# Performance work log

Measured on AMD Instinct MI355X. Metric: run time of the kernel, lower is better.

## Reference

```python
import jax, jax.numpy as jnp
import numpy as np

N_NODES = 100000
N_EDGES = 1600000
F_IN = 256
F_OUT = 32


def setup_inputs() -> dict:
    key = jax.random.key(0)
    k1, k2, k3 = jax.random.split(key, 3)
    x = jax.random.normal(k1, (N_NODES, F_IN), dtype=jnp.float32)
    edge_index = jax.random.randint(k2, (2, N_EDGES), 0, N_NODES, dtype=jnp.int64)
    W = jax.random.normal(k3, (F_IN, F_OUT), dtype=jnp.float32) / np.sqrt(F_IN)
    b = jnp.zeros((F_OUT,), dtype=jnp.float32)
    return {"x": x, "edge_index": edge_index, "W": W, "b": b}


def reference(x, edge_index, W, b):
    # PyG GCNConv: add self-loops, symmetric normalization, linear, aggregate.
    N = x.shape[0]
    loop = jnp.arange(N, dtype=edge_index.dtype)
    src = jnp.concatenate([edge_index[0], loop])  # message sources
    dst = jnp.concatenate([edge_index[1], loop])  # aggregation targets

    deg = jax.ops.segment_sum(jnp.ones_like(dst, dtype=x.dtype), dst,
                              num_segments=N)
    deg_inv_sqrt = jnp.where(deg > 0, jax.lax.rsqrt(jnp.maximum(deg, 1.0)), 0.0)
    norm = deg_inv_sqrt[src] * deg_inv_sqrt[dst]  # [E+N]

    h = x @ W  # [N, F_OUT] transform first (as PyG does)
    msg = h[src] * norm[:, None]  # gather + scale
    out = jax.ops.segment_sum(msg, dst, num_segments=N) + b
    return out
```

## Files before the change

### kernel.cpp

```cpp
#include <hip/hip_runtime.h>

#define F_IN  256
#define F_OUT 32

#define NPB       512
#define NPB_SHIFT 9
#define NB2MAX    256
#define EPW       8192
#define BCAP      10240

typedef __attribute__((ext_vector_type(8))) short bf16x8;
typedef __attribute__((ext_vector_type(4))) float f32x4;

__device__ __forceinline__ short f2bf(float f) {
    unsigned u = __float_as_uint(f);
    u += 0x7FFF + ((u >> 16) & 1);
    return (short)(u >> 16);
}

__global__ __launch_bounds__(256) void k_zero(int* __restrict__ bcur,
                                              const int* __restrict__ ei,
                                              int* __restrict__ flag) {
    int i = blockIdx.x * 256 + threadIdx.x;
    if (i < NB2MAX) bcur[i] = i * BCAP;
    if (i == 0) {
        int o = 0;
        for (int k = 1; k < 64; k += 2) o |= ei[k];
        *flag = (o == 0) ? 1 : 0;
    }
}

__global__ __launch_bounds__(512) void k_bucket(const int* __restrict__ ei,
                                                const int* __restrict__ flag,
                                                int* __restrict__ bcur,
                                                int* __restrict__ ebuf,
                                                int E, int N) {
    __shared__ int lhist[NB2MAX];
    __shared__ int lbase[NB2MAX];
    __shared__ int sP[EPW];
    __shared__ unsigned short sB[EPW];
    const int tid = threadIdx.x;
    if (tid < NB2MAX) lhist[tid] = 0;
    __syncthreads();
    const int m64 = *flag;
    const long long e0 = (long long)blockIdx.x * EPW;
    #pragma unroll 4
    for (int j = 0; j < EPW / 512; ++j) {
        int idx = j * 512 + tid;
        long long e = e0 + idx;
        unsigned short bb = 0xFFFF;
        int pk = 0;
        if (e < E) {
            int s, d;
            if (m64) { s = ei[2 * (size_t)e]; d = ei[2 * ((size_t)E + e)]; }
            else     { s = ei[(size_t)e];     d = ei[(size_t)E + e]; }
            if ((unsigned)d < (unsigned)N && (unsigned)s < (unsigned)N) {
                bb = (unsigned short)(d >> NPB_SHIFT);
                pk = s | ((d & (NPB - 1)) << 23);
                atomicAdd(&lhist[bb], 1);
            }
        }
        sB[idx] = bb;
        sP[idx] = pk;
    }
    __syncthreads();
    if (tid < NB2MAX) {
        int c = lhist[tid];
        lbase[tid] = c ? atomicAdd(&bcur[tid], c) : 0;
        lhist[tid] = 0;
    }
    __syncthreads();
    #pragma unroll 4
    for (int j = 0; j < EPW / 512; ++j) {
        int idx = j * 512 + tid;
        unsigned short bb = sB[idx];
        if (bb != 0xFFFF) {
            int slot = lbase[bb] + atomicAdd(&lhist[bb], 1);
            if (slot < (int)(bb + 1) * BCAP) ebuf[slot] = sP[idx];
        }
    }
}

__global__ __launch_bounds__(1024) void k_sort(int* __restrict__ ebuf,
                                               const int* __restrict__ bcur,
                                               float* __restrict__ dinv,
                                               int* __restrict__ offp, int N) {
    __shared__ int sedge[BCAP];
    __shared__ int lcnt[NPB];
    __shared__ int lofs[NPB];
    __shared__ int sc[NPB];
    const int tid = threadIdx.x;
    const int b = blockIdx.x;
    const int start = b * BCAP;
    const int m = min(max(bcur[b] - start, 0), BCAP);

    for (int i = tid; i < m; i += 1024) sedge[i] = ebuf[start + i];
    if (tid < NPB) lcnt[tid] = 0;
    __syncthreads();
    for (int i = tid; i < m; i += 1024)
        atomicAdd(&lcnt[((unsigned)sedge[i]) >> 23], 1);
    __syncthreads();
    int c0 = (tid < NPB) ? lcnt[tid] : 0;
    int val = c0;
    if (tid < NPB) sc[tid] = val;
    __syncthreads();
    #pragma unroll
    for (int d2 = 1; d2 < NPB; d2 <<= 1) {
        int t = (tid < NPB && tid >= d2) ? sc[tid - d2] : 0;
        __syncthreads();
        if (tid < NPB) { val += t; sc[tid] = val; }
        __syncthreads();
    }
    if (tid < NPB) {
        int excl = val - c0;
        lofs[tid] = excl;
        int n = (b << NPB_SHIFT) + tid;
        if (n < N) {
            dinv[n] = rsqrtf((float)c0 + 1.0f);
            offp[n] = (start + excl) | (min(c0, 1023) << 22);
        }
    }
    __syncthreads();
    for (int i = tid; i < m; i += 1024) {
        int pk = sedge[i];
        int l = ((unsigned)pk) >> 23;
        int slot = start + atomicAdd(&lofs[l], 1);
        ebuf[slot] = pk & 0x7FFFFF;
    }
}

#define WLDP 264
__global__ __launch_bounds__(256) void k_gemm(const float* __restrict__ x,
                                              const float* __restrict__ W,
                                              const float* __restrict__ dinv,
                                              _Float16* __restrict__ hs16, int N) {
    __shared__ __align__(16) short sWt[F_OUT * WLDP];
    const int tid = threadIdx.x;
    const int lane = tid & 63;
    const int wave = tid >> 6;
    const int row0 = blockIdx.x * 128 + wave * 32;

    for (int i = tid; i < F_IN * F_OUT; i += 256) {
        int f = i & 31, k = i >> 5;
        sWt[f * WLDP + k] = f2bf(W[i]);
    }
    __syncthreads();

    const int l15 = lane & 15;
    const int lg  = lane >> 4;
    int ra = row0 + l15;
    int rb = row0 + 16 + l15;
    int rac = min(ra, N - 1);
    int rbc = min(rb, N - 1);

    const float* xa = x + (size_t)rac * F_IN + lg * 8;
    const float* xb = x + (size_t)rbc * F_IN + lg * 8;
    const short* wb0 = sWt + l15 * WLDP + lg * 8;
    const short* wb1 = sWt + (16 + l15) * WLDP + lg * 8;

    f32x4 acc00 = {0.f, 0.f, 0.f, 0.f};
    f32x4 acc01 = {0.f, 0.f, 0.f, 0.f};
    f32x4 acc10 = {0.f, 0.f, 0.f, 0.f};
    f32x4 acc11 = {0.f, 0.f, 0.f, 0.f};

    #pragma unroll
    for (int kb = 0; kb < F_IN / 32; ++kb) {
        float4 a0 = *(const float4*)(xa + kb * 32);
        float4 a1 = *(const float4*)(xa + kb * 32 + 4);
        float4 b0 = *(const float4*)(xb + kb * 32);
        float4 b1 = *(const float4*)(xb + kb * 32 + 4);
        bf16x8 A0, A1;
        A0[0] = f2bf(a0.x); A0[1] = f2bf(a0.y); A0[2] = f2bf(a0.z); A0[3] = f2bf(a0.w);
        A0[4] = f2bf(a1.x); A0[5] = f2bf(a1.y); A0[6] = f2bf(a1.z); A0[7] = f2bf(a1.w);
        A1[0] = f2bf(b0.x); A1[1] = f2bf(b0.y); A1[2] = f2bf(b0.z); A1[3] = f2bf(b0.w);
        A1[4] = f2bf(b1.x); A1[5] = f2bf(b1.y); A1[6] = f2bf(b1.z); A1[7] = f2bf(b1.w);
        bf16x8 B0 = *(const bf16x8*)(wb0 + kb * 32);
        bf16x8 B1 = *(const bf16x8*)(wb1 + kb * 32);
        acc00 = __builtin_amdgcn_mfma_f32_16x16x32_bf16(A0, B0, acc00, 0, 0, 0);
        acc01 = __builtin_amdgcn_mfma_f32_16x16x32_bf16(A0, B1, acc01, 0, 0, 0);
        acc10 = __builtin_amdgcn_mfma_f32_16x16x32_bf16(A1, B0, acc10, 0, 0, 0);
        acc11 = __builtin_amdgcn_mfma_f32_16x16x32_bf16(A1, B1, acc11, 0, 0, 0);
    }

    #pragma unroll
    for (int r = 0; r < 4; ++r) {
        int row = row0 + lg * 4 + r;
        if (row < N) {
            float di = dinv[row];
            hs16[(size_t)row * F_OUT + l15]      = (_Float16)(acc00[r] * di);
            hs16[(size_t)row * F_OUT + 16 + l15] = (_Float16)(acc01[r] * di);
        }
        int row2 = row + 16;
        if (row2 < N) {
            float di2 = dinv[row2];
            hs16[(size_t)row2 * F_OUT + l15]      = (_Float16)(acc10[r] * di2);
            hs16[(size_t)row2 * F_OUT + 16 + l15] = (_Float16)(acc11[r] * di2);
        }
    }
}

__global__ __launch_bounds__(256) void k_agg(const _Float16* __restrict__ hs16,
                                             const int* __restrict__ adj,
                                             const int* __restrict__ offp,
                                             const float* __restrict__ dinv,
                                             const float* __restrict__ bias,
                                             float* __restrict__ out, int N) {
    const int tid = threadIdx.x;
    const int n = blockIdx.x * 64 + (tid >> 2);
    const int q = tid & 3;
    if (n >= N) return;

    const int po = offp[n];
    const int st = po & 0x3FFFFF;
    const int deg = ((unsigned)po) >> 22;

    const uint4* __restrict__ h4 = (const uint4*)hs16;
    union U { uint4 u; _Float16 h[8]; };

    float a[8];
    {
        U sv; sv.u = h4[(size_t)n * 4 + q];
        #pragma unroll
        for (int i = 0; i < 8; ++i) a[i] = (float)sv.h[i];
    }

    int k = 0;
    for (; k + 4 <= deg; k += 4) {
        int s0 = adj[st + k];
        int s1 = adj[st + k + 1];
        int s2 = adj[st + k + 2];
        int s3 = adj[st + k + 3];
        U v0, v1, v2, v3;
        v0.u = h4[(size_t)s0 * 4 + q];
        v1.u = h4[(size_t)s1 * 4 + q];
        v2.u = h4[(size_t)s2 * 4 + q];
        v3.u = h4[(size_t)s3 * 4 + q];
        #pragma unroll
        for (int i = 0; i < 8; ++i)
            a[i] += ((float)v0.h[i] + (float)v1.h[i]) +
                    ((float)v2.h[i] + (float)v3.h[i]);
    }
    for (; k < deg; ++k) {
        int s0 = adj[st + k];
        U v0; v0.u = h4[(size_t)s0 * 4 + q];
        #pragma unroll
        for (int i = 0; i < 8; ++i) a[i] += (float)v0.h[i];
    }

    const float di = dinv[n];
    const float4 bv0 = ((const float4*)bias)[q * 2];
    const float4 bv1 = ((const float4*)bias)[q * 2 + 1];
    float4 o0, o1;
    o0.x = bv0.x + di * a[0]; o0.y = bv0.y + di * a[1];
    o0.z = bv0.z + di * a[2]; o0.w = bv0.w + di * a[3];
    o1.x = bv1.x + di * a[4]; o1.y = bv1.y + di * a[5];
    o1.z = bv1.z + di * a[6]; o1.w = bv1.w + di * a[7];
    float4* op = (float4*)(out + (size_t)n * F_OUT);
    op[q * 2]     = o0;
    op[q * 2 + 1] = o1;
}

extern "C" void kernel_launch(void* const* d_in, const int* in_sizes, int n_in,
                              void* d_out, int out_size, void* d_ws, size_t ws_size,
                              hipStream_t stream) {
    const float* x  = (const float*)d_in[0];
    const int*   ei = (const int*)d_in[1];
    const float* W  = (const float*)d_in[2];
    const float* b  = (const float*)d_in[3];
    float* out = (float*)d_out;

    const int N = in_sizes[0] / F_IN;
    const int E = in_sizes[1] / 2;

    _Float16* hs16 = (_Float16*)d_ws;
    int*   ebuf = (int*)(hs16 + (size_t)N * F_OUT);
    float* dinv = (float*)(ebuf + (size_t)NB2MAX * BCAP);
    int*   offp = (int*)(dinv + N);
    int*   bcur = offp + N;
    int*   flag = bcur + NB2MAX;

    const int NB  = (N + NPB - 1) >> NPB_SHIFT;
    const int NBW = (int)(((long long)E + EPW - 1) / EPW);

    k_zero  <<<1, 256, 0, stream>>>(bcur, ei, flag);
    k_bucket<<<NBW, 512, 0, stream>>>(ei, flag, bcur, ebuf, E, N);
    k_sort  <<<NB, 1024, 0, stream>>>(ebuf, bcur, dinv, offp, N);
    k_gemm  <<<(N + 127) / 128, 256, 0, stream>>>(x, W, dinv, hs16, N);
    k_agg   <<<(N * 4 + 255) / 256, 256, 0, stream>>>(hs16, ebuf, offp, dinv, b, out, N);
}
```

Baseline: 231.4 us.

## Sort nodes by degree within blocks and unroll aggregation by eight

k_sort now builds a per-block counting sort of nodes by in-degree and writes a node permutation (nord). k_agg walks nodes in that order, so neighbouring threads and waves handle nodes of similar degree, which reduces loop-trip divergence inside a wave. The aggregation loop also gains an 8-wide unroll with a second accumulator set, giving more gathers in flight. The cost is an extra indirection load per node, scattered output writes, and extra scans and atomics in k_sort plus a larger k_zero launch.

```diff
diff --git a/kernel.cpp b/kernel.cpp
--- a/kernel.cpp
+++ b/kernel.cpp
@@ -8,6 +8,7 @@
 #define NB2MAX    256
 #define EPW       8192
 #define BCAP      10240
+#define DEGB      128
 
 typedef __attribute__((ext_vector_type(8))) short bf16x8;
 typedef __attribute__((ext_vector_type(4))) float f32x4;
@@ -19,10 +20,12 @@
 }
 
 __global__ __launch_bounds__(256) void k_zero(int* __restrict__ bcur,
+                                              int* __restrict__ nord,
                                               const int* __restrict__ ei,
-                                              int* __restrict__ flag) {
+                                              int* __restrict__ flag, int tot) {
     int i = blockIdx.x * 256 + threadIdx.x;
     if (i < NB2MAX) bcur[i] = i * BCAP;
+    if (i < tot) nord[i] = -1;
     if (i == 0) {
         int o = 0;
         for (int k = 1; k < 64; k += 2) o |= ei[k];
@@ -84,11 +87,14 @@
 __global__ __launch_bounds__(1024) void k_sort(int* __restrict__ ebuf,
                                                const int* __restrict__ bcur,
                                                float* __restrict__ dinv,
-                                               int* __restrict__ offp, int N) {
+                                               int* __restrict__ offp,
+                                               int* __restrict__ nord, int N) {
     __shared__ int sedge[BCAP];
     __shared__ int lcnt[NPB];
     __shared__ int lofs[NPB];
     __shared__ int sc[NPB];
+    __shared__ int dh[DEGB];
+    __shared__ int dho[DEGB];
     const int tid = threadIdx.x;
     const int b = blockIdx.x;
     const int start = b * BCAP;
@@ -96,6 +102,7 @@
 
     for (int i = tid; i < m; i += 1024) sedge[i] = ebuf[start + i];
     if (tid < NPB) lcnt[tid] = 0;
+    if (tid >= NPB && tid < NPB + DEGB) dh[tid - NPB] = 0;
     __syncthreads();
     for (int i = tid; i < m; i += 1024)
         atomicAdd(&lcnt[((unsigned)sedge[i]) >> 23], 1);
@@ -111,16 +118,37 @@
         if (tid < NPB) { val += t; sc[tid] = val; }
         __syncthreads();
     }
+    const int n = (b << NPB_SHIFT) + tid;
+    const int nvalid = (tid < NPB) && (n < N);
     if (tid < NPB) {
         int excl = val - c0;
         lofs[tid] = excl;
-        int n = (b << NPB_SHIFT) + tid;
-        if (n < N) {
+        if (nvalid) {
             dinv[n] = rsqrtf((float)c0 + 1.0f);
             offp[n] = (start + excl) | (min(c0, 1023) << 22);
         }
     }
     __syncthreads();
+    const int dg = min(c0, DEGB - 1);
+    if (nvalid) atomicAdd(&dh[dg], 1);
+    __syncthreads();
+    int dv = (tid < DEGB) ? dh[tid] : 0;
+    int dval = dv;
+    if (tid < DEGB) sc[tid] = dval;
+    __syncthreads();
+    #pragma unroll
+    for (int d2 = 1; d2 < DEGB; d2 <<= 1) {
+        int t = (tid < DEGB && tid >= d2) ? sc[tid - d2] : 0;
+        __syncthreads();
+        if (tid < DEGB) { dval += t; sc[tid] = dval; }
+        __syncthreads();
+    }
+    if (tid < DEGB) dho[tid] = dval - dv;
+    __syncthreads();
+    if (nvalid) {
+        int r = atomicAdd(&dho[dg], 1);
+        nord[(b << NPB_SHIFT) + r] = n;
+    }
     for (int i = tid; i < m; i += 1024) {
         int pk = sedge[i];
         int l = ((unsigned)pk) >> 23;
@@ -202,13 +230,16 @@
 __global__ __launch_bounds__(256) void k_agg(const _Float16* __restrict__ hs16,
                                              const int* __restrict__ adj,
                                              const int* __restrict__ offp,
+                                             const int* __restrict__ nord,
                                              const float* __restrict__ dinv,
                                              const float* __restrict__ bias,
-                                             float* __restrict__ out, int N) {
+                                             float* __restrict__ out, int N, int tot) {
     const int tid = threadIdx.x;
-    const int n = blockIdx.x * 64 + (tid >> 2);
+    const int r = blockIdx.x * 64 + (tid >> 2);
     const int q = tid & 3;
-    if (n >= N) return;
+    if (r >= tot) return;
+    const int n = nord[r];
+    if ((unsigned)n >= (unsigned)N) return;
 
     const int po = offp[n];
     const int st = po & 0x3FFFFF;
@@ -217,14 +248,40 @@
     const uint4* __restrict__ h4 = (const uint4*)hs16;
     union U { uint4 u; _Float16 h[8]; };
 
-    float a[8];
+    float a[8], c[8];
     {
         U sv; sv.u = h4[(size_t)n * 4 + q];
         #pragma unroll
-        for (int i = 0; i < 8; ++i) a[i] = (float)sv.h[i];
+        for (int i = 0; i < 8; ++i) { a[i] = (float)sv.h[i]; c[i] = 0.f; }
     }
 
     int k = 0;
+    for (; k + 8 <= deg; k += 8) {
+        int s0 = adj[st + k];
+        int s1 = adj[st + k + 1];
+        int s2 = adj[st + k + 2];
+        int s3 = adj[st + k + 3];
+        int s4 = adj[st + k + 4];
+        int s5 = adj[st + k + 5];
+        int s6 = adj[st + k + 6];
+        int s7 = adj[st + k + 7];
+        U v0, v1, v2, v3, v4, v5, v6, v7;
+        v0.u = h4[(size_t)s0 * 4 + q];
+        v1.u = h4[(size_t)s1 * 4 + q];
+        v2.u = h4[(size_t)s2 * 4 + q];
+        v3.u = h4[(size_t)s3 * 4 + q];
+        v4.u = h4[(size_t)s4 * 4 + q];
+        v5.u = h4[(size_t)s5 * 4 + q];
+        v6.u = h4[(size_t)s6 * 4 + q];
+        v7.u = h4[(size_t)s7 * 4 + q];
+        #pragma unroll
+        for (int i = 0; i < 8; ++i) {
+            a[i] += ((float)v0.h[i] + (float)v1.h[i]) +
+                    ((float)v2.h[i] + (float)v3.h[i]);
+            c[i] += ((float)v4.h[i] + (float)v5.h[i]) +
+                    ((float)v6.h[i] + (float)v7.h[i]);
+        }
+    }
     for (; k + 4 <= deg; k += 4) {
         int s0 = adj[st + k];
         int s1 = adj[st + k + 1];
@@ -251,10 +308,10 @@
     const float4 bv0 = ((const float4*)bias)[q * 2];
     const float4 bv1 = ((const float4*)bias)[q * 2 + 1];
     float4 o0, o1;
-    o0.x = bv0.x + di * a[0]; o0.y = bv0.y + di * a[1];
-    o0.z = bv0.z + di * a[2]; o0.w = bv0.w + di * a[3];
-    o1.x = bv1.x + di * a[4]; o1.y = bv1.y + di * a[5];
-    o1.z = bv1.z + di * a[6]; o1.w = bv1.w + di * a[7];
+    o0.x = bv0.x + di * (a[0] + c[0]); o0.y = bv0.y + di * (a[1] + c[1]);
+    o0.z = bv0.z + di * (a[2] + c[2]); o0.w = bv0.w + di * (a[3] + c[3]);
+    o1.x = bv1.x + di * (a[4] + c[4]); o1.y = bv1.y + di * (a[5] + c[5]);
+    o1.z = bv1.z + di * (a[6] + c[6]); o1.w = bv1.w + di * (a[7] + c[7]);
     float4* op = (float4*)(out + (size_t)n * F_OUT);
     op[q * 2]     = o0;
     op[q * 2 + 1] = o1;
@@ -276,15 +333,17 @@
     int*   ebuf = (int*)(hs16 + (size_t)N * F_OUT);
     float* dinv = (float*)(ebuf + (size_t)NB2MAX * BCAP);
     int*   offp = (int*)(dinv + N);
-    int*   bcur = offp + N;
+    int*   nord = offp + N;
+    int*   bcur = nord + (size_t)NB2MAX * NPB;
     int*   flag = bcur + NB2MAX;
 
     const int NB  = (N + NPB - 1) >> NPB_SHIFT;
     const int NBW = (int)(((long long)E + EPW - 1) / EPW);
-
-    k_zero  <<<1, 256, 0, stream>>>(bcur, ei, flag);
+    const int tot = NB * NPB;
+
+    k_zero  <<<(tot + 255) / 256, 256, 0, stream>>>(bcur, nord, ei, flag, tot);
     k_bucket<<<NBW, 512, 0, stream>>>(ei, flag, bcur, ebuf, E, N);
-    k_sort  <<<NB, 1024, 0, stream>>>(ebuf, bcur, dinv, offp, N);
+    k_sort  <<<NB, 1024, 0, stream>>>(ebuf, bcur, dinv, offp, nord, N);
     k_gemm  <<<(N + 127) / 128, 256, 0, stream>>>(x, W, dinv, hs16, N);
-    k_agg   <<<(N * 4 + 255) / 256, 256, 0, stream>>>(hs16, ebuf, offp, dinv, b, out, N);
-}
+    k_agg   <<<(tot * 4 + 255) / 256, 256, 0, stream>>>(hs16, ebuf, offp, nord, dinv, b, out, N, tot);
+}
```

After: 244.6 us. +5.7%, slower.
